# Kernel tuning notes

Hardware: AMD Instinct MI355X
Metric: run time of the kernel (lower is better)

Reference implementation:

```python
import jax, jax.numpy as jnp
import numpy as np

B, S, D, H = 16, 512, 512, 8
DH = D // H
EPS = 1e-5
NEG = -1.0e9


def _layernorm(v, g, b):
    mu = jnp.mean(v, axis=-1, keepdims=True)
    var = jnp.mean(jnp.square(v - mu), axis=-1, keepdims=True)
    return (v - mu) * jax.lax.rsqrt(var + EPS) * g + b


def setup_inputs() -> dict:
    key = jax.random.key(0)
    ks = jax.random.split(key, 12)
    sd = 1.0 / np.sqrt(D)
    return {
        "x": jax.random.normal(ks[0], (B, S, D), dtype=jnp.float32),
        "mask": jax.random.randint(ks[1], (B, S, S), 0, 2, dtype=jnp.int32),
        "ln_g": jnp.ones((D,), jnp.float32),
        "ln_b": jnp.zeros((D,), jnp.float32),
        "lna_g": jnp.ones((S,), jnp.float32),  # LayerNorm over attention scores (last dim = S = model_dim)
        "lna_b": jnp.zeros((S,), jnp.float32),
        "Wq": jax.random.uniform(ks[2], (D, D), jnp.float32, -sd, sd),
        "bq": jnp.zeros((D,), jnp.float32),
        "Wk": jax.random.uniform(ks[3], (D, D), jnp.float32, -sd, sd),
        "bk": jnp.zeros((D,), jnp.float32),
        "Wv": jax.random.uniform(ks[4], (D, D), jnp.float32, -sd, sd),
        "bv": jnp.zeros((D,), jnp.float32),
        "Wd": jax.random.uniform(ks[5], (D, D), jnp.float32, -sd, sd),
        "bd": jnp.zeros((D,), jnp.float32),
    }


def reference(x, mask, ln_g, ln_b, lna_g, lna_b, Wq, bq, Wk, bk, Wv, bv, Wd, bd):
    # pre-LN
    h = _layernorm(x, ln_g, ln_b)  # [B,S,D]
    # projections -> [B,H,S,DH]
    q = (h @ Wq + bq).reshape(B, S, H, DH).transpose(0, 2, 1, 3)
    k = (h @ Wk + bk).reshape(B, S, H, DH).transpose(0, 2, 1, 3)
    v = (h @ Wv + bv).reshape(B, S, H, DH).transpose(0, 2, 1, 3)
    # raw scores [B,H,S,S]
    scores = jnp.einsum("bhqd,bhkd->bhqk", q, k) / jnp.sqrt(jnp.asarray(DH, x.dtype))
    # non-standard: LayerNorm over the key axis of the score matrix
    scores = _layernorm(scores, lna_g, lna_b)
    # mask (broadcast over heads), then softmax
    scores = jnp.where(mask[:, None, :, :] == 0, jnp.asarray(NEG, x.dtype), scores)
    attn = jax.nn.softmax(scores, axis=-1)
    # dropout omitted (eval mode / deterministic reference)
    out = jnp.einsum("bhqk,bhkd->bhqd", attn, v)
    out = out.transpose(0, 2, 1, 3).reshape(B, S, D)
    out = out @ Wd + bd
    return out + x
```

## Files before the change

### kernel.cpp

```cpp
#include <hip/hip_runtime.h>
#include <hip/hip_bf16.h>
#include <stdint.h>


typedef __hip_bfloat16 bf16;
typedef __bf16 bf16x8 __attribute__((ext_vector_type(8)));
typedef float f32x4 __attribute__((ext_vector_type(4)));

#define MFMA16(a, b, c) __builtin_amdgcn_mfma_f32_16x16x32_bf16((a), (b), (c), 0, 0, 0)

static __device__ __forceinline__ bf16 f2b(float v) { return __float2bfloat16(v); }
static __device__ __forceinline__ bf16x8 ld8(const bf16* p) { return *(const bf16x8*)p; }
static __device__ __forceinline__ uint16_t f2bu(float v) {
  return __hip_bfloat16_raw(__float2bfloat16(v)).x;
}
static __device__ __forceinline__ float bu2f(uint32_t u) {
  union { uint32_t i; float f; } c;
  c.i = u << 16;
  return c.f;
}
static __device__ __forceinline__ void stage16(const bf16* g, bf16* l) {
  __builtin_amdgcn_global_load_lds(
      (const __attribute__((address_space(1))) void*)g,
      (__attribute__((address_space(3))) void*)l, 16, 0, 0);
}

__global__ __launch_bounds__(256) void prep(
    const float* __restrict__ x, const float* __restrict__ lng,
    const float* __restrict__ lnb, bf16* __restrict__ h,
    const int* __restrict__ mask, uint32_t* __restrict__ bits,
    const float* __restrict__ W0, const float* __restrict__ W1,
    const float* __restrict__ W2, const float* __restrict__ W3,
    bf16* __restrict__ T0, bf16* __restrict__ T1,
    bf16* __restrict__ T2, bf16* __restrict__ T3) {
  __shared__ float t[32][33];
  __shared__ float rs[4], rs2[4];
  const int bid = blockIdx.x;
  const int tid = threadIdx.x;

  if (bid < 8192) {
    int row = bid;
    const float* xr = x + (size_t)row * 512;
    float v0 = xr[tid], v1 = xr[tid + 256];
    float s = v0 + v1, s2 = v0 * v0 + v1 * v1;
#pragma unroll
    for (int m = 1; m < 64; m <<= 1) {
      s += __shfl_xor(s, m);
      s2 += __shfl_xor(s2, m);
    }
    int w = tid >> 6;
    if ((tid & 63) == 0) { rs[w] = s; rs2[w] = s2; }
    __syncthreads();
    s = rs[0] + rs[1] + rs[2] + rs[3];
    s2 = rs2[0] + rs2[1] + rs2[2] + rs2[3];
    float mean = s * (1.0f / 512.0f);
    float var = s2 * (1.0f / 512.0f) - mean * mean;
    float rstd = rsqrtf(var + 1e-5f);
    bf16* hr = h + (size_t)row * 512;
    hr[tid] = f2b((v0 - mean) * rstd * lng[tid] + lnb[tid]);
    hr[tid + 256] = f2b((v1 - mean) * rstd * lng[tid + 256] + lnb[tid + 256]);
  } else if (bid < 24576) {
    size_t e = (size_t)(bid - 8192) * 256 + tid;
    int mv = mask[e];
    unsigned long long bal = __ballot(mv != 0);
    if ((tid & 63) == 0) ((unsigned long long*)bits)[e >> 6] = bal;
  } else {
    int tt = bid - 24576;
    int wsel = tt >> 8, rem = tt & 255;
    int n0 = (rem & 15) * 32, k0 = (rem >> 4) * 32;
    const float* src; bf16* dst;
    switch (wsel) {
      case 0: src = W0; dst = T0; break;
      case 1: src = W1; dst = T1; break;
      case 2: src = W2; dst = T2; break;
      default: src = W3; dst = T3; break;
    }
    int tx = tid & 31, ty = tid >> 5;
#pragma unroll
    for (int i = 0; i < 4; i++) {
      int kk = ty * 4 + i;
      t[kk][tx] = src[(k0 + kk) * 512 + n0 + tx];
    }
    __syncthreads();
#pragma unroll
    for (int i = 0; i < 4; i++) {
      int nn = ty * 4 + i;
      dst[(n0 + nn) * 512 + k0 + tx] = f2b(t[tx][nn]);
    }
  }
}

__global__ __launch_bounds__(256) void gemm_qkv(
    const bf16* __restrict__ hm,
    const bf16* __restrict__ WT0, const bf16* __restrict__ WT1, const bf16* __restrict__ WT2,
    const float* __restrict__ bq, const float* __restrict__ bk, const float* __restrict__ bv,
    bf16* __restrict__ outq, bf16* __restrict__ outk, bf16* __restrict__ outvT) {
  const int sel = blockIdx.z;
  const bf16* WT = sel == 0 ? WT0 : (sel == 1 ? WT1 : WT2);
  const float* bias = sel == 0 ? bq : (sel == 1 ? bk : bv);
  __shared__ __align__(16) uint16_t SM[128 * 136];
  bf16* As = (bf16*)SM;
  bf16* Bs = (bf16*)(SM + 4096);
  int tid = threadIdx.x;
  int w = tid >> 6, lane = tid & 63, q4 = lane >> 4, l16 = lane & 15;
  int wr = w >> 1, wc = w & 1;
  int m0 = blockIdx.x * 128, n0 = blockIdx.y * 128;
  f32x4 acc[4][4];
#pragma unroll
  for (int i = 0; i < 4; i++)
#pragma unroll
    for (int j = 0; j < 4; j++) acc[i][j] = (f32x4){0.f, 0.f, 0.f, 0.f};

  for (int kc = 0; kc < 16; kc++) {
    int k0 = kc * 32;
#pragma unroll
    for (int u0 = 0; u0 < 2; u0++) {
      int e = u0 * 256 + tid;
      int row = e >> 2, c8 = (e & 3) * 8;
      stage16(&hm[(size_t)(m0 + row) * 512 + k0 + c8], &As[e * 8]);
      stage16(&WT[(size_t)(n0 + row) * 512 + k0 + c8], &Bs[e * 8]);
    }
    __syncthreads();
    bf16x8 af[4], bfr[4];
#pragma unroll
    for (int rt = 0; rt < 4; rt++)
      af[rt] = ld8(&As[(wr * 64 + rt * 16 + l16) * 32 + q4 * 8]);
#pragma unroll
    for (int nt = 0; nt < 4; nt++)
      bfr[nt] = ld8(&Bs[(wc * 64 + nt * 16 + l16) * 32 + q4 * 8]);
#pragma unroll
    for (int rt = 0; rt < 4; rt++)
#pragma unroll
      for (int nt = 0; nt < 4; nt++) acc[rt][nt] = MFMA16(af[rt], bfr[nt], acc[rt][nt]);
    __syncthreads();
  }

  if (sel != 2) {
    const float scale = sel == 0 ? 0.125f : 1.0f;
#pragma unroll
    for (int rt = 0; rt < 4; rt++)
#pragma unroll
      for (int nt = 0; nt < 4; nt++) {
        int ncol = wc * 64 + nt * 16 + l16;
        float bsv = bias[n0 + ncol];
#pragma unroll
        for (int r = 0; r < 4; r++) {
          int mrow = wr * 64 + rt * 16 + q4 * 4 + r;
          SM[mrow * 136 + ncol] = f2bu((acc[rt][nt][r] + bsv) * scale);
        }
      }
    __syncthreads();
    bf16* dst = sel == 0 ? outq : outk;
#pragma unroll
    for (int p = 0; p < 8; p++) {
      int e = p * 256 + tid;
      int row = e >> 4, c8 = (e & 15) * 8;
      bf16x8 vv = *(bf16x8*)&SM[row * 136 + c8];
      int gm = m0 + row, b_ = gm >> 9, s_ = gm & 511;
      int n = n0 + c8, hh = n >> 6, dh = n & 63;
      *(bf16x8*)(dst + ((size_t)((b_ * 8 + hh) * 512 + s_)) * 64 + dh) = vv;
    }
  } else {
#pragma unroll
    for (int rt = 0; rt < 4; rt++)
#pragma unroll
      for (int nt = 0; nt < 4; nt++) {
        int ncol = wc * 64 + nt * 16 + l16;
        float bsv = bias[n0 + ncol];
        union { uint16_t q[4]; uint2 u; } pk;
#pragma unroll
        for (int r = 0; r < 4; r++) pk.q[r] = f2bu(acc[rt][nt][r] + bsv);
        *(uint2*)&SM[ncol * 136 + wr * 64 + rt * 16 + q4 * 4] = pk.u;
      }
    __syncthreads();
#pragma unroll
    for (int p = 0; p < 8; p++) {
      int e = p * 256 + tid;
      int nn = e >> 4, s8 = (e & 15) * 8;
      bf16x8 vv = *(bf16x8*)&SM[nn * 136 + s8];
      int n = n0 + nn, hh = n >> 6, dh = n & 63;
      int gm = m0 + s8, b_ = gm >> 9, s_ = gm & 511;
      *(bf16x8*)(outvT + ((size_t)((b_ * 8 + hh) * 64 + dh)) * 512 + s_) = vv;
    }
  }
}

__global__ __launch_bounds__(256, 4) void attn_fused(
    const bf16* __restrict__ q, const bf16* __restrict__ k, const bf16* __restrict__ vT,
    const uint32_t* __restrict__ bits, const float* __restrict__ lg,
    const float* __restrict__ lb, bf16* __restrict__ ctx) {
  const int id = blockIdx.x;
  const int xcd = id & 7;
  const int j = id >> 3;
  const int mt = j & 7;
  const int bh = ((j >> 3) << 3) | xcd;
  const int m0 = mt * 64;
  const int b = bh >> 3, hh = bh & 7;
  const int tid = threadIdx.x;
  const int w = tid >> 6, lane = tid & 63, q4 = lane >> 4, l16 = lane & 15;

  __shared__ __align__(16) bf16 SBk[2][32 * 72];
  __shared__ __align__(16) bf16 SBv[2][64 * 40];
  __shared__ uint32_t GB[512];
  __shared__ uint32_t sbits[64][17];

  GB[tid] = (uint32_t)f2bu(lg[tid]) | ((uint32_t)f2bu(lb[tid]) << 16);
  GB[tid + 256] = (uint32_t)f2bu(lg[tid + 256]) | ((uint32_t)f2bu(lb[tid + 256]) << 16);
  {
    int row = tid >> 2, g = tid & 3;
    const uint32_t* src = bits + ((size_t)b * 512 + m0 + row) * 16 + g * 4;
    uint4 u = *(const uint4*)src;
    sbits[row][g * 4] = u.x; sbits[row][g * 4 + 1] = u.y;
    sbits[row][g * 4 + 2] = u.z; sbits[row][g * 4 + 3] = u.w;
  }

  const bf16* qb = q + ((size_t)bh * 512 + m0 + w * 16) * 64;
  const bf16* kb = k + (size_t)bh * 512 * 64;
  const bf16* vb = vT + (size_t)bh * 64 * 512;

  bf16x8 aq0 = ld8(qb + (size_t)l16 * 64 + q4 * 8);
  bf16x8 aq1 = ld8(qb + (size_t)l16 * 64 + 32 + q4 * 8);

  {
    int key0 = tid >> 3, dh8 = (tid & 7) * 8;
    *(bf16x8*)&SBk[0][key0 * 72 + dh8] = ld8(kb + (size_t)key0 * 64 + dh8);
  }
  __syncthreads();

  float s = 0.f, s2 = 0.f;
  for (int c = 0; c < 16; c++) {
    const int buf = c & 1;
    if (c < 15) {
      int key0 = tid >> 3, dh8 = (tid & 7) * 8;
      *(bf16x8*)&SBk[buf ^ 1][key0 * 72 + dh8] =
          ld8(kb + (size_t)((c + 1) * 32 + key0) * 64 + dh8);
    }
#pragma unroll
    for (int kg = 0; kg < 2; kg++) {
      const bf16* kp = &SBk[buf][(kg * 16 + l16) * 72];
      bf16x8 b0 = ld8(kp + q4 * 8);
      bf16x8 b1 = ld8(kp + 32 + q4 * 8);
      f32x4 acc = (f32x4){0.f, 0.f, 0.f, 0.f};
      acc = MFMA16(b0, aq0, acc);
      acc = MFMA16(b1, aq1, acc);
#pragma unroll
      for (int r = 0; r < 4; r++) {
        float v = acc[r];
        s += v;
        s2 += v * v;
      }
    }
    __syncthreads();
  }
  s += __shfl_xor(s, 16);  s += __shfl_xor(s, 32);
  s2 += __shfl_xor(s2, 16); s2 += __shfl_xor(s2, 32);
  const float mean = s * (1.0f / 512.0f);
  const float rstd = rsqrtf(s2 * (1.0f / 512.0f) - mean * mean + 1e-5f);

  {
    int key0 = tid >> 3, dh8 = (tid & 7) * 8;
    *(bf16x8*)&SBk[0][key0 * 72 + dh8] = ld8(kb + (size_t)key0 * 64 + dh8);
    int dh = tid >> 2, kk8 = (tid & 3) * 8;
    *(bf16x8*)&SBv[0][dh * 40 + kk8] = ld8(vb + (size_t)dh * 512 + kk8);
  }
  __syncthreads();

  f32x4 o[4];
#pragma unroll
  for (int nt = 0; nt < 4; nt++) o[nt] = (f32x4){0.f, 0.f, 0.f, 0.f};
  float se = 0.f;
  const int src0 = ((q4 & 1) * 2) * 16 + l16;
  const int src1 = src0 + 16;
  const bool hi = (q4 >> 1) != 0;

  for (int c = 0; c < 16; c++) {
    const int buf = c & 1;
    if (c < 15) {
      int key0 = tid >> 3, dh8 = (tid & 7) * 8;
      *(bf16x8*)&SBk[buf ^ 1][key0 * 72 + dh8] =
          ld8(kb + (size_t)((c + 1) * 32 + key0) * 64 + dh8);
      int dh = tid >> 2, kk8 = (tid & 3) * 8;
      *(bf16x8*)&SBv[buf ^ 1][dh * 40 + kk8] =
          ld8(vb + (size_t)dh * 512 + (c + 1) * 32 + kk8);
    }
    const uint32_t dw = sbits[w * 16 + l16][c];
    uint32_t Pk[2][2];
#pragma unroll
    for (int kg = 0; kg < 2; kg++) {
      const bf16* kp = &SBk[buf][(kg * 16 + l16) * 72];
      bf16x8 b0 = ld8(kp + q4 * 8);
      bf16x8 b1 = ld8(kp + 32 + q4 * 8);
      f32x4 acc = (f32x4){0.f, 0.f, 0.f, 0.f};
      acc = MFMA16(b0, aq0, acc);
      acc = MFMA16(b1, aq1, acc);
      uint4 gb4 = *(uint4*)&GB[c * 32 + kg * 16 + q4 * 4];
      uint16_t p[4];
#pragma unroll
      for (int r = 0; r < 4; r++) {
        uint32_t gb = r == 0 ? gb4.x : (r == 1 ? gb4.y : (r == 2 ? gb4.z : gb4.w));
        float t = (acc[r] - mean) * rstd * bu2f(gb & 0xffffu) + bu2f(gb >> 16);
        t = ((dw >> (kg * 16 + q4 * 4 + r)) & 1u) ? t : -1.0e9f;
        float pf = __expf(t);
        se += pf;
        p[r] = f2bu(pf);
      }
      Pk[kg][0] = (uint32_t)p[0] | ((uint32_t)p[1] << 16);
      Pk[kg][1] = (uint32_t)p[2] | ((uint32_t)p[3] << 16);
    }
    uint32_t t00 = __shfl(Pk[0][0], src0), t01 = __shfl(Pk[1][0], src0);
    uint32_t t10 = __shfl(Pk[0][1], src0), t11 = __shfl(Pk[1][1], src0);
    uint32_t t20 = __shfl(Pk[0][0], src1), t21 = __shfl(Pk[1][0], src1);
    uint32_t t30 = __shfl(Pk[0][1], src1), t31 = __shfl(Pk[1][1], src1);
    union { uint32_t d[4]; bf16x8 v; } af;
    af.d[0] = hi ? t01 : t00;
    af.d[1] = hi ? t11 : t10;
    af.d[2] = hi ? t21 : t20;
    af.d[3] = hi ? t31 : t30;
#pragma unroll
    for (int nt = 0; nt < 4; nt++) {
      bf16x8 bv8 = ld8(&SBv[buf][(nt * 16 + l16) * 40 + q4 * 8]);
      o[nt] = MFMA16(af.v, bv8, o[nt]);
    }
    __syncthreads();
  }

  se += __shfl_xor(se, 16);
  se += __shfl_xor(se, 32);
  float invr = 1.0f / se;
  float inv[4];
#pragma unroll
  for (int r = 0; r < 4; r++) inv[r] = __shfl(invr, q4 * 4 + r);

  bf16* cb = ctx + ((size_t)b * 512 + m0 + w * 16) * 512 + hh * 64;
#pragma unroll
  for (int nt = 0; nt < 4; nt++)
#pragma unroll
    for (int r = 0; r < 4; r++)
      cb[(size_t)(q4 * 4 + r) * 512 + nt * 16 + l16] = f2b(o[nt][r] * inv[r]);
}

__global__ __launch_bounds__(256) void gemm_out(
    const bf16* __restrict__ ctx, const bf16* __restrict__ WT,
    const float* __restrict__ bd, const float* __restrict__ x, float* __restrict__ out) {
  __shared__ __align__(16) bf16 As[64 * 32];
  __shared__ __align__(16) bf16 Bs[128 * 32];
  int tid = threadIdx.x;
  int w = tid >> 6, lane = tid & 63, q4 = lane >> 4, l16 = lane & 15;
  int m0 = blockIdx.x * 64, n0 = blockIdx.y * 128;
  f32x4 acc[4][2];
#pragma unroll
  for (int i = 0; i < 4; i++)
#pragma unroll
    for (int j = 0; j < 2; j++) acc[i][j] = (f32x4){0.f, 0.f, 0.f, 0.f};

  for (int kc = 0; kc < 16; kc++) {
    int k0 = kc * 32;
    {
      int e = tid;
      int row = e >> 2, c8 = (e & 3) * 8;
      stage16(&ctx[(size_t)(m0 + row) * 512 + k0 + c8], &As[e * 8]);
    }
#pragma unroll
    for (int u0 = 0; u0 < 2; u0++) {
      int e = u0 * 256 + tid;
      int row = e >> 2, c8 = (e & 3) * 8;
      stage16(&WT[(size_t)(n0 + row) * 512 + k0 + c8], &Bs[e * 8]);
    }
    __syncthreads();
    bf16x8 af[4], bfr[2];
#pragma unroll
    for (int rt = 0; rt < 4; rt++)
      af[rt] = ld8(&As[(rt * 16 + l16) * 32 + q4 * 8]);
#pragma unroll
    for (int nt = 0; nt < 2; nt++)
      bfr[nt] = ld8(&Bs[(w * 32 + nt * 16 + l16) * 32 + q4 * 8]);
#pragma unroll
    for (int rt = 0; rt < 4; rt++)
#pragma unroll
      for (int nt = 0; nt < 2; nt++) acc[rt][nt] = MFMA16(af[rt], bfr[nt], acc[rt][nt]);
    __syncthreads();
  }
#pragma unroll
  for (int rt = 0; rt < 4; rt++) {
    int mbase = m0 + rt * 16 + q4 * 4;
#pragma unroll
    for (int nt = 0; nt < 2; nt++) {
      int n = n0 + w * 32 + nt * 16 + l16;
      float bsv = bd[n];
#pragma unroll
      for (int r = 0; r < 4; r++) {
        size_t idx = (size_t)(mbase + r) * 512 + n;
        out[idx] = acc[rt][nt][r] + bsv + x[idx];
      }
    }
  }
}

extern "C" void kernel_launch(void* const* d_in, const int* in_sizes, int n_in,
                              void* d_out, int out_size, void* d_ws, size_t ws_size,
                              hipStream_t stream) {
  const float* x = (const float*)d_in[0];
  const int* mask = (const int*)d_in[1];
  const float* ln_g = (const float*)d_in[2];
  const float* ln_b = (const float*)d_in[3];
  const float* lna_g = (const float*)d_in[4];
  const float* lna_b = (const float*)d_in[5];
  const float* Wq = (const float*)d_in[6];
  const float* bq = (const float*)d_in[7];
  const float* Wk = (const float*)d_in[8];
  const float* bk = (const float*)d_in[9];
  const float* Wv = (const float*)d_in[10];
  const float* bv = (const float*)d_in[11];
  const float* Wd = (const float*)d_in[12];
  const float* bd = (const float*)d_in[13];

  char* ws = (char*)d_ws;
  const size_t MB = 1024 * 1024;
  if (ws_size < 44 * MB) return;
  bf16* h = (bf16*)(ws);
  bf16* qd = (bf16*)(ws + 8 * MB);
  bf16* kd = (bf16*)(ws + 16 * MB);
  bf16* vTd = (bf16*)(ws + 24 * MB);
  bf16* ctx = (bf16*)(ws + 32 * MB);
  bf16* WqT = (bf16*)(ws + 40 * MB);
  bf16* WkT = (bf16*)(ws + 40 * MB + 512 * 1024);
  bf16* WvT = (bf16*)(ws + 40 * MB + 1024 * 1024);
  bf16* WdT = (bf16*)(ws + 40 * MB + 1536 * 1024);
  uint32_t* bits = (uint32_t*)(ws + 42 * MB);

  prep<<<25600, 256, 0, stream>>>(x, ln_g, ln_b, h, mask, bits,
                                  Wq, Wk, Wv, Wd, WqT, WkT, WvT, WdT);
  gemm_qkv<<<dim3(64, 4, 3), 256, 0, stream>>>(h, WqT, WkT, WvT, bq, bk, bv, qd, kd, vTd);
  attn_fused<<<1024, 256, 0, stream>>>(qd, kd, vTd, bits, lna_g, lna_b, ctx);
  gemm_out<<<dim3(128, 4), 256, 0, stream>>>(ctx, WdT, bd, x, (float*)d_out);
}
```

Measured before the change: 177.8 us.

## Compute score LayerNorm stats algebraically via K^T K Gram matrix kernel

Removes the first QK^T pass in the attention kernel that computed per-row mean and variance of scores. A new attn_stats kernel builds the per-head Gram matrix K^T K and the key-sum vector, using hi/lo bf16 splits to keep precision, then gets each row's sum as q·sum(k) and its sum of squares as q^T M q. The QKV GEMM now also writes a transposed K for this. The attention loop additionally prefetches the next K/V chunk into registers and stores it to LDS after the PV MFMAs, to overlap the loads. The cost is an extra launch, an extra K^T write, and some numerical risk from the E[x^2]-E[x]^2 form.

After: 194.2 us. +9.2%, slower.

```diff
diff --git a/kernel.cpp b/kernel.cpp
--- a/kernel.cpp
+++ b/kernel.cpp
@@ -94,7 +94,8 @@
     const bf16* __restrict__ hm,
     const bf16* __restrict__ WT0, const bf16* __restrict__ WT1, const bf16* __restrict__ WT2,
     const float* __restrict__ bq, const float* __restrict__ bk, const float* __restrict__ bv,
-    bf16* __restrict__ outq, bf16* __restrict__ outk, bf16* __restrict__ outvT) {
+    bf16* __restrict__ outq, bf16* __restrict__ outk, bf16* __restrict__ outvT,
+    bf16* __restrict__ outkT) {
   const int sel = blockIdx.z;
   const bf16* WT = sel == 0 ? WT0 : (sel == 1 ? WT1 : WT2);
   const float* bias = sel == 0 ? bq : (sel == 1 ? bk : bv);
@@ -149,6 +150,23 @@
           SM[mrow * 136 + ncol] = f2bu((acc[rt][nt][r] + bsv) * scale);
         }
       }
+    if (sel == 1) {
+#pragma unroll
+      for (int rt = 0; rt < 4; rt++) {
+        int gm = m0 + wr * 64 + rt * 16 + q4 * 4;
+        int b_ = gm >> 9, s_ = gm & 511;
+#pragma unroll
+        for (int nt = 0; nt < 4; nt++) {
+          int ncol = wc * 64 + nt * 16 + l16;
+          int n = n0 + ncol, hh = n >> 6, dh = n & 63;
+          float bsv = bias[n0 + ncol];
+          union { uint16_t q[4]; uint2 u; } pk;
+#pragma unroll
+          for (int r = 0; r < 4; r++) pk.q[r] = f2bu(acc[rt][nt][r] + bsv);
+          *(uint2*)(outkT + ((size_t)((b_ * 8 + hh) * 64 + dh)) * 512 + s_) = pk.u;
+        }
+      }
+    }
     __syncthreads();
     bf16* dst = sel == 0 ? outq : outk;
 #pragma unroll
@@ -185,10 +203,113 @@
   }
 }
 
+__global__ __launch_bounds__(256) void attn_stats(
+    const bf16* __restrict__ q, const bf16* __restrict__ kT,
+    float2* __restrict__ st) {
+  const int bh = blockIdx.x >> 1;
+  const int half = blockIdx.x & 1;
+  const int tid = threadIdx.x;
+  const int w = tid >> 6, lane = tid & 63, q4 = lane >> 4, l16 = lane & 15;
+  const bf16* kb = kT + (size_t)bh * 64 * 512;
+  const bf16* qb = q + (size_t)bh * 512 * 64;
+
+  __shared__ __align__(16) uint16_t Mhi[64][72];
+  __shared__ __align__(16) uint16_t Mlo[64][72];
+  __shared__ __align__(16) uint16_t KbH[64], KbL[64];
+
+  union { uint16_t u[8]; bf16x8 v; } ones;
+#pragma unroll
+  for (int i = 0; i < 8; i++) ones.u[i] = 0x3F80;
+
+  f32x4 mac[4];
+  f32x4 kac = (f32x4){0.f, 0.f, 0.f, 0.f};
+#pragma unroll
+  for (int jt = 0; jt < 4; jt++) mac[jt] = (f32x4){0.f, 0.f, 0.f, 0.f};
+  for (int kc = 0; kc < 16; kc++) {
+    bf16x8 a = ld8(&kb[(size_t)(w * 16 + l16) * 512 + kc * 32 + q4 * 8]);
+#pragma unroll
+    for (int jt = 0; jt < 4; jt++) {
+      bf16x8 b = ld8(&kb[(size_t)(jt * 16 + l16) * 512 + kc * 32 + q4 * 8]);
+      mac[jt] = MFMA16(a, b, mac[jt]);
+    }
+    kac = MFMA16(a, ones.v, kac);
+  }
+#pragma unroll
+  for (int jt = 0; jt < 4; jt++)
+#pragma unroll
+    for (int r = 0; r < 4; r++) {
+      float m = mac[jt][r];
+      uint16_t hi = f2bu(m);
+      Mhi[w * 16 + q4 * 4 + r][jt * 16 + l16] = hi;
+      Mlo[w * 16 + q4 * 4 + r][jt * 16 + l16] = f2bu(m - bu2f(hi));
+    }
+  if (l16 == 0) {
+#pragma unroll
+    for (int r = 0; r < 4; r++) {
+      float v = kac[r];
+      uint16_t hi = f2bu(v);
+      KbH[w * 16 + q4 * 4 + r] = hi;
+      KbL[w * 16 + q4 * 4 + r] = f2bu(v - bu2f(hi));
+    }
+  }
+  __syncthreads();
+
+  const int rbase = half * 256 + w * 64;
+#pragma unroll 1
+  for (int rt = 0; rt < 4; rt++) {
+    const int row0 = rbase + rt * 16;
+    f32x4 tac[4];
+    f32x4 mn = (f32x4){0.f, 0.f, 0.f, 0.f};
+#pragma unroll
+    for (int jt = 0; jt < 4; jt++) tac[jt] = (f32x4){0.f, 0.f, 0.f, 0.f};
+#pragma unroll
+    for (int ic = 0; ic < 2; ic++) {
+      bf16x8 aq = ld8(&qb[(size_t)(row0 + l16) * 64 + ic * 32 + q4 * 8]);
+#pragma unroll
+      for (int jt = 0; jt < 4; jt++) {
+        bf16x8 bh_ = *(const bf16x8*)&Mhi[jt * 16 + l16][ic * 32 + q4 * 8];
+        tac[jt] = MFMA16(aq, bh_, tac[jt]);
+        bf16x8 bl_ = *(const bf16x8*)&Mlo[jt * 16 + l16][ic * 32 + q4 * 8];
+        tac[jt] = MFMA16(aq, bl_, tac[jt]);
+      }
+      bf16x8 kh = *(const bf16x8*)&KbH[ic * 32 + q4 * 8];
+      mn = MFMA16(aq, kh, mn);
+      bf16x8 kl = *(const bf16x8*)&KbL[ic * 32 + q4 * 8];
+      mn = MFMA16(aq, kl, mn);
+    }
+    float s2p[4];
+#pragma unroll
+    for (int r = 0; r < 4; r++) {
+      const int qrow = row0 + q4 * 4 + r;
+      float acc = 0.f;
+#pragma unroll
+      for (int jt = 0; jt < 4; jt++) {
+        float qv = __bfloat162float(qb[(size_t)qrow * 64 + jt * 16 + l16]);
+        acc += tac[jt][r] * qv;
+      }
+      acc += __shfl_xor(acc, 1);
+      acc += __shfl_xor(acc, 2);
+      acc += __shfl_xor(acc, 4);
+      acc += __shfl_xor(acc, 8);
+      s2p[r] = acc;
+    }
+    if (l16 == 0) {
+#pragma unroll
+      for (int r = 0; r < 4; r++) {
+        const int qrow = row0 + q4 * 4 + r;
+        float mean = mn[r] * (1.0f / 512.0f);
+        float var = s2p[r] * (1.0f / 512.0f) - mean * mean;
+        st[(size_t)bh * 512 + qrow] = make_float2(mean, rsqrtf(var + 1e-5f));
+      }
+    }
+  }
+}
+
 __global__ __launch_bounds__(256, 4) void attn_fused(
     const bf16* __restrict__ q, const bf16* __restrict__ k, const bf16* __restrict__ vT,
-    const uint32_t* __restrict__ bits, const float* __restrict__ lg,
-    const float* __restrict__ lb, bf16* __restrict__ ctx) {
+    const uint32_t* __restrict__ bits, const float2* __restrict__ st,
+    const float* __restrict__ lg, const float* __restrict__ lb,
+    bf16* __restrict__ ctx) {
   const int id = blockIdx.x;
   const int xcd = id & 7;
   const int j = id >> 3;
@@ -221,48 +342,13 @@
   bf16x8 aq0 = ld8(qb + (size_t)l16 * 64 + q4 * 8);
   bf16x8 aq1 = ld8(qb + (size_t)l16 * 64 + 32 + q4 * 8);
 
-  {
-    int key0 = tid >> 3, dh8 = (tid & 7) * 8;
-    *(bf16x8*)&SBk[0][key0 * 72 + dh8] = ld8(kb + (size_t)key0 * 64 + dh8);
-  }
-  __syncthreads();
-
-  float s = 0.f, s2 = 0.f;
-  for (int c = 0; c < 16; c++) {
-    const int buf = c & 1;
-    if (c < 15) {
-      int key0 = tid >> 3, dh8 = (tid & 7) * 8;
-      *(bf16x8*)&SBk[buf ^ 1][key0 * 72 + dh8] =
-          ld8(kb + (size_t)((c + 1) * 32 + key0) * 64 + dh8);
-    }
-#pragma unroll
-    for (int kg = 0; kg < 2; kg++) {
-      const bf16* kp = &SBk[buf][(kg * 16 + l16) * 72];
-      bf16x8 b0 = ld8(kp + q4 * 8);
-      bf16x8 b1 = ld8(kp + 32 + q4 * 8);
-      f32x4 acc = (f32x4){0.f, 0.f, 0.f, 0.f};
-      acc = MFMA16(b0, aq0, acc);
-      acc = MFMA16(b1, aq1, acc);
-#pragma unroll
-      for (int r = 0; r < 4; r++) {
-        float v = acc[r];
-        s += v;
-        s2 += v * v;
-      }
-    }
-    __syncthreads();
-  }
-  s += __shfl_xor(s, 16);  s += __shfl_xor(s, 32);
-  s2 += __shfl_xor(s2, 16); s2 += __shfl_xor(s2, 32);
-  const float mean = s * (1.0f / 512.0f);
-  const float rstd = rsqrtf(s2 * (1.0f / 512.0f) - mean * mean + 1e-5f);
-
-  {
-    int key0 = tid >> 3, dh8 = (tid & 7) * 8;
-    *(bf16x8*)&SBk[0][key0 * 72 + dh8] = ld8(kb + (size_t)key0 * 64 + dh8);
-    int dh = tid >> 2, kk8 = (tid & 3) * 8;
-    *(bf16x8*)&SBv[0][dh * 40 + kk8] = ld8(vb + (size_t)dh * 512 + kk8);
-  }
+  const float2 ms = st[(size_t)bh * 512 + m0 + w * 16 + l16];
+  const float mean = ms.x, rstd = ms.y;
+
+  const int key0 = tid >> 3, dh8 = (tid & 7) * 8;
+  const int dhv = tid >> 2, kk8 = (tid & 3) * 8;
+  *(bf16x8*)&SBk[0][key0 * 72 + dh8] = ld8(kb + (size_t)key0 * 64 + dh8);
+  *(bf16x8*)&SBv[0][dhv * 40 + kk8] = ld8(vb + (size_t)dhv * 512 + kk8);
   __syncthreads();
 
   f32x4 o[4];
@@ -275,13 +361,10 @@
 
   for (int c = 0; c < 16; c++) {
     const int buf = c & 1;
+    bf16x8 rk, rv;
     if (c < 15) {
-      int key0 = tid >> 3, dh8 = (tid & 7) * 8;
-      *(bf16x8*)&SBk[buf ^ 1][key0 * 72 + dh8] =
-          ld8(kb + (size_t)((c + 1) * 32 + key0) * 64 + dh8);
-      int dh = tid >> 2, kk8 = (tid & 3) * 8;
-      *(bf16x8*)&SBv[buf ^ 1][dh * 40 + kk8] =
-          ld8(vb + (size_t)dh * 512 + (c + 1) * 32 + kk8);
+      rk = ld8(kb + (size_t)((c + 1) * 32 + key0) * 64 + dh8);
+      rv = ld8(vb + (size_t)dhv * 512 + (c + 1) * 32 + kk8);
     }
     const uint32_t dw = sbits[w * 16 + l16][c];
     uint32_t Pk[2][2];
@@ -320,6 +403,10 @@
     for (int nt = 0; nt < 4; nt++) {
       bf16x8 bv8 = ld8(&SBv[buf][(nt * 16 + l16) * 40 + q4 * 8]);
       o[nt] = MFMA16(af.v, bv8, o[nt]);
+    }
+    if (c < 15) {
+      *(bf16x8*)&SBk[buf ^ 1][key0 * 72 + dh8] = rk;
+      *(bf16x8*)&SBv[buf ^ 1][dhv * 40 + kk8] = rv;
     }
     __syncthreads();
   }
@@ -416,7 +503,7 @@
 
   char* ws = (char*)d_ws;
   const size_t MB = 1024 * 1024;
-  if (ws_size < 44 * MB) return;
+  if (ws_size < 53 * MB) return;
   bf16* h = (bf16*)(ws);
   bf16* qd = (bf16*)(ws + 8 * MB);
   bf16* kd = (bf16*)(ws + 16 * MB);
@@ -427,10 +514,14 @@
   bf16* WvT = (bf16*)(ws + 40 * MB + 1024 * 1024);
   bf16* WdT = (bf16*)(ws + 40 * MB + 1536 * 1024);
   uint32_t* bits = (uint32_t*)(ws + 42 * MB);
+  bf16* kTd = (bf16*)(ws + 44 * MB);
+  float2* st = (float2*)(ws + 52 * MB);
 
   prep<<<25600, 256, 0, stream>>>(x, ln_g, ln_b, h, mask, bits,
                                   Wq, Wk, Wv, Wd, WqT, WkT, WvT, WdT);
-  gemm_qkv<<<dim3(64, 4, 3), 256, 0, stream>>>(h, WqT, WkT, WvT, bq, bk, bv, qd, kd, vTd);
-  attn_fused<<<1024, 256, 0, stream>>>(qd, kd, vTd, bits, lna_g, lna_b, ctx);
+  gemm_qkv<<<dim3(64, 4, 3), 256, 0, stream>>>(h, WqT, WkT, WvT, bq, bk, bv,
+                                               qd, kd, vTd, kTd);
+  attn_stats<<<256, 256, 0, stream>>>(qd, kTd, st);
+  attn_fused<<<1024, 256, 0, stream>>>(qd, kd, vTd, bits, st, lna_g, lna_b, ctx);
   gemm_out<<<dim3(128, 4), 256, 0, stream>>>(ctx, WdT, bd, x, (float*)d_out);
 }
```
